# Optimization experiments

Measured on AMD Instinct MI355X. Metric: run time of the kernel, lower is better.

Reference implementation:

```python
import jax, jax.numpy as jnp
import numpy as np

B, NS, NF, T, D = 64, 2, 13, 24, 512
H = 8
DH = D // H
DFF = 2048
EPS = 1e-5


def setup_inputs() -> dict:
    key = jax.random.key(0)
    ks = jax.random.split(key, 16)
    s = 0.02
    inp = {
        'x': jax.random.normal(ks[0], (B, NS * NF, T, D), jnp.float32),
        'w_in_s': jax.random.normal(ks[1], (3 * D, D), jnp.float32) * s,
        'b_in_s': jnp.zeros((3 * D,), jnp.float32),
        'w_out_s': jax.random.normal(ks[2], (D, D), jnp.float32) * s,
        'b_out_s': jnp.zeros((D,), jnp.float32),
        'w_in_f': jax.random.normal(ks[3], (3 * D, D), jnp.float32) * s,
        'b_in_f': jnp.zeros((3 * D,), jnp.float32),
        'w_out_f': jax.random.normal(ks[4], (D, D), jnp.float32) * s,
        'b_out_f': jnp.zeros((D,), jnp.float32),
        'w1': jax.random.normal(ks[5], (DFF, D), jnp.float32) * s,
        'b1': jnp.zeros((DFF,), jnp.float32),
        'w2': jax.random.normal(ks[6], (D, DFF), jnp.float32) * s,
        'b2': jnp.zeros((D,), jnp.float32),
        'g1': jnp.ones((D,), jnp.float32), 'be1': jnp.zeros((D,), jnp.float32),
        'g2': jnp.ones((D,), jnp.float32), 'be2': jnp.zeros((D,), jnp.float32),
        'g3': jnp.ones((D,), jnp.float32), 'be3': jnp.zeros((D,), jnp.float32),
    }
    return inp


def _layer_norm(x, g, b):
    mu = jnp.mean(x, axis=-1, keepdims=True)
    var = jnp.mean(jnp.square(x - mu), axis=-1, keepdims=True)
    return (x - mu) * jax.lax.rsqrt(var + EPS) * g + b


def _mha(x, w_in, b_in, w_out, b_out):
    # x: [..., S, D]; torch nn.MultiheadAttention math, eval mode (no dropout)
    qkv = x @ w_in.T + b_in                     # [..., S, 3D]
    q, k, v = jnp.split(qkv, 3, axis=-1)
    shp = q.shape[:-1] + (H, DH)
    q, k, v = q.reshape(shp), k.reshape(shp), v.reshape(shp)
    scores = jnp.einsum('...qhd,...khd->...hqk', q, k) / np.sqrt(DH).astype(np.float32)
    a = jax.nn.softmax(scores, axis=-1)
    o = jnp.einsum('...hqk,...khd->...qhd', a, v).reshape(x.shape)
    return o @ w_out.T + b_out


def reference(x, w_in_s, b_in_s, w_out_s, b_out_s, w_in_f, b_in_f, w_out_f, b_out_f,
              w1, b1, w2, b2, g1, be1, g2, be2, g3, be3):
    xr = x.reshape(B, NS, NF, T, D)
    # station attention: attend over the NS axis for each (feature, t)
    xs = xr.transpose(0, 2, 3, 1, 4)            # [B, NF, T, NS, D]
    xs = xs + _mha(xs, w_in_s, b_in_s, w_out_s, b_out_s)
    x = xs.transpose(0, 3, 1, 2, 4).reshape(B, NS * NF, T, D)
    x = _layer_norm(x, g1, be1)
    # feature attention: attend over the NF axis for each (station, t)
    xr = x.reshape(B, NS, NF, T, D)
    xf = xr.transpose(0, 1, 3, 2, 4)            # [B, NS, T, NF, D]
    xf = xf + _mha(xf, w_in_f, b_in_f, w_out_f, b_out_f)
    x = xf.transpose(0, 1, 3, 2, 4).reshape(B, NS * NF, T, D)
    x = _layer_norm(x, g2, be2)
    # feed-forward
    ff = jax.nn.relu(x @ w1.T + b1) @ w2.T + b2
    x = _layer_norm(x + ff, g3, be3)
    return x
```

## Files before the change

kernel.cpp:

```cpp
#include <hip/hip_runtime.h>
#include <stdint.h>

typedef unsigned short u16;
typedef __bf16 bf16x8 __attribute__((ext_vector_type(8)));
typedef float f32x4 __attribute__((ext_vector_type(4)));

#define DEV __device__ __forceinline__

DEV float bf2f(u16 u) {
    union { uint32_t u; float f; } c; c.u = ((uint32_t)u) << 16; return c.f;
}
DEV u16 f2bf(float f) {
    union { float f; uint32_t u; } c; c.f = f;
    uint32_t u = c.u;
    u += 0x7FFFu + ((u >> 16) & 1u);
    return (u16)(u >> 16);
}

DEV void gload_lds16(const u16* gp, u16* lp) {
    __builtin_amdgcn_global_load_lds(
        (__attribute__((address_space(1))) u16*)(uintptr_t)gp,
        (__attribute__((address_space(3))) u16*)lp,
        16, 0, 0);
}

#define WAITVM6 asm volatile("s_waitcnt vmcnt(6)" ::: "memory")
#define WAITVM4 asm volatile("s_waitcnt vmcnt(4)" ::: "memory")
#define WAITVM0 asm volatile("s_waitcnt vmcnt(0)" ::: "memory")
#define MEMFENCE asm volatile("" ::: "memory")

DEV void load16f(const u16* p, float* f) {
    uint4 a = *reinterpret_cast<const uint4*>(p);
    uint4 b = *reinterpret_cast<const uint4*>(p + 8);
    uint32_t w[8] = { a.x, a.y, a.z, a.w, b.x, b.y, b.z, b.w };
#pragma unroll
    for (int k = 0; k < 8; ++k) {
        union { uint32_t u; float f; } lo, hi;
        lo.u = w[k] << 16; hi.u = w[k] & 0xFFFF0000u;
        f[2 * k] = lo.f; f[2 * k + 1] = hi.f;
    }
}
DEV float dot16(const u16* p, const float* q) {
    uint4 a = *reinterpret_cast<const uint4*>(p);
    uint4 b = *reinterpret_cast<const uint4*>(p + 8);
    uint32_t w[8] = { a.x, a.y, a.z, a.w, b.x, b.y, b.z, b.w };
    float d = 0.0f;
#pragma unroll
    for (int k = 0; k < 8; ++k) {
        union { uint32_t u; float f; } lo, hi;
        lo.u = w[k] << 16; hi.u = w[k] & 0xFFFF0000u;
        d += q[2 * k] * lo.f;
        d += q[2 * k + 1] * hi.f;
    }
    return d;
}
DEV void fma16(const u16* p, float pw, float* acc) {
    uint4 a = *reinterpret_cast<const uint4*>(p);
    uint4 b = *reinterpret_cast<const uint4*>(p + 8);
    uint32_t w[8] = { a.x, a.y, a.z, a.w, b.x, b.y, b.z, b.w };
#pragma unroll
    for (int k = 0; k < 8; ++k) {
        union { uint32_t u; float f; } lo, hi;
        lo.u = w[k] << 16; hi.u = w[k] & 0xFFFF0000u;
        acc[2 * k] += pw * lo.f;
        acc[2 * k + 1] += pw * hi.f;
    }
}
DEV void store16(u16* p, const float* y) {
    uint32_t w[8];
#pragma unroll
    for (int k = 0; k < 8; ++k)
        w[k] = (uint32_t)f2bf(y[2 * k]) | ((uint32_t)f2bf(y[2 * k + 1]) << 16);
    uint4 a = { w[0], w[1], w[2], w[3] };
    uint4 b = { w[4], w[5], w[6], w[7] };
    *reinterpret_cast<uint4*>(p) = a;
    *reinterpret_cast<uint4*>(p + 8) = b;
}

__global__ __launch_bounds__(256) void k_f32_to_bf16(
    const float* __restrict__ in, u16* __restrict__ out, int n4)
{
    int i = blockIdx.x * 256 + threadIdx.x;
    if (i >= n4) return;
    float4 v = reinterpret_cast<const float4*>(in)[i];
    ushort4 o;
    o.x = f2bf(v.x); o.y = f2bf(v.y); o.z = f2bf(v.z); o.w = f2bf(v.w);
    reinterpret_cast<ushort4*>(out)[i] = o;
}

__global__ __launch_bounds__(256) void k_convw(
    const float* __restrict__ s0, const float* __restrict__ s1,
    const float* __restrict__ s2, const float* __restrict__ s3,
    const float* __restrict__ s4, const float* __restrict__ s5,
    u16* __restrict__ out)
{
    const int i = blockIdx.x * 256 + threadIdx.x;
    const float4* src;
    int off;
    if      (i <  196608) { src = (const float4*)s0; off = i; }
    else if (i <  262144) { src = (const float4*)s1; off = i - 196608; }
    else if (i <  458752) { src = (const float4*)s2; off = i - 262144; }
    else if (i <  524288) { src = (const float4*)s3; off = i - 458752; }
    else if (i <  786432) { src = (const float4*)s4; off = i - 524288; }
    else                  { src = (const float4*)s5; off = i - 786432; }
    float4 v = src[off];
    ushort4 o;
    o.x = f2bf(v.x); o.y = f2bf(v.y); o.z = f2bf(v.z); o.w = f2bf(v.w);
    reinterpret_cast<ushort4*>(out)[i] = o;
}

template<bool RELU, bool RESID, int NT>
__global__ __launch_bounds__(512, 2) void k_gemm8p(
    const u16* __restrict__ A, const u16* __restrict__ W,
    const float* __restrict__ bias, const u16* __restrict__ res,
    u16* __restrict__ C, int M, int N, int K)
{
    __shared__ __align__(16) u16 Abuf[2][16384];
    __shared__ __align__(16) u16 Bbuf[2][16384];

    const int tid  = threadIdx.x;
    const int lane = tid & 63;
    const int wave = tid >> 6;
    const int wm   = wave >> 2;
    const int wn   = wave & 3;
    const int l15  = lane & 15;
    const int lg   = lane >> 4;

    const int nwg = gridDim.x;
    const int v = (blockIdx.x & 7) * (nwg >> 3) + (blockIdx.x >> 3);
    const long tileM = (long)(v / NT) * 256;
    const long tileN = (long)(v % NT) * 256;

    const int nIter = K >> 7;

    f32x4 acc[8][4] = {};

    const long Abase = (tileM + (tid >> 3)) * (long)K + (((tid & 7) ^ ((tid >> 3) & 7)) << 3);
    const long Bbase = (tileN + (tid >> 3)) * (long)K + (((tid & 7) ^ ((tid >> 3) & 7)) << 3);

    auto stA = [&](int h, int t) {
#pragma unroll
        for (int e = 0; e < 2; ++e)
            gload_lds16(A + Abase + (long)(h * 128 + e * 64) * K + t * 64,
                        &Abuf[t & 1][(h * 1024 + e * 512 + tid) * 8]);
    };
    auto stB = [&](int h, int t) {
#pragma unroll
        for (int e = 0; e < 2; ++e)
            gload_lds16(W + Bbase + (long)(h * 128 + e * 64) * K + t * 64,
                        &Bbuf[t & 1][(h * 1024 + e * 512 + tid) * 8]);
    };

    int koff[2];
#pragma unroll
    for (int ks = 0; ks < 2; ++ks)
        koff[ks] = ((ks * 4 + lg) ^ (l15 & 7)) * 8;
    const int aRow = wm * 128 + l15;
    const int bRow = wn * 64 + l15;

    stA(0, 0); stA(1, 0); stB(0, 0); stB(1, 0); stB(0, 1); stB(1, 1);
    WAITVM4;
    MEMFENCE;
    __builtin_amdgcn_s_barrier();
    MEMFENCE;

    bf16x8 b[4][2];

    for (int j = 0; j < nIter; ++j) {
        const bool pre = (j + 1 < nIter);
        const int E = 2 * j;
#pragma unroll
        for (int ph = 0; ph < 8; ++ph) {
            const int bb = ph >> 2;
            const int q  = ph & 3;
            if (q == 0) {
#pragma unroll
                for (int n = 0; n < 4; ++n)
#pragma unroll
                    for (int ks = 0; ks < 2; ++ks)
                        b[n][ks] = *reinterpret_cast<const bf16x8*>(
                            &Bbuf[bb][(bRow + n * 16) * 64 + koff[ks]]);
            }
            bf16x8 aq[2][2];
#pragma unroll
            for (int mi = 0; mi < 2; ++mi)
#pragma unroll
                for (int ks = 0; ks < 2; ++ks)
                    aq[mi][ks] = *reinterpret_cast<const bf16x8*>(
                        &Abuf[bb][(aRow + (q * 2 + mi) * 16) * 64 + koff[ks]]);
            if (ph == 0) stA(0, E + 1);
            else if (ph == 1) stA(1, E + 1);
            else if (ph == 2) { if (pre) stB(0, E + 2); }
            else if (ph == 3) {
                if (pre) { stB(1, E + 2); WAITVM4; } else { WAITVM0; }
            }
            else if (ph == 4) { if (pre) stA(0, E + 2); }
            else if (ph == 5) { if (pre) stA(1, E + 2); }
            else if (ph == 6) { if (pre) stB(0, E + 3); }
            else {
                if (pre) { stB(1, E + 3); WAITVM4; } else { WAITVM0; }
            }
            MEMFENCE;
            __builtin_amdgcn_s_barrier();
            MEMFENCE;
            __builtin_amdgcn_s_setprio(1);
#pragma unroll
            for (int mi = 0; mi < 2; ++mi)
#pragma unroll
                for (int n = 0; n < 4; ++n)
#pragma unroll
                    for (int ks = 0; ks < 2; ++ks)
                        acc[q * 2 + mi][n] = __builtin_amdgcn_mfma_f32_16x16x32_bf16(
                            aq[mi][ks], b[n][ks], acc[q * 2 + mi][n], 0, 0, 0);
            __builtin_amdgcn_s_setprio(0);
            MEMFENCE;
            __builtin_amdgcn_s_barrier();
            MEMFENCE;
        }
    }

    const int crow0 = (int)tileM + wm * 128 + ((lane >> 4) << 2);
    const int ccol0 = (int)tileN + wn * 64 + l15;
#pragma unroll
    for (int m = 0; m < 8; ++m) {
#pragma unroll
        for (int n = 0; n < 4; ++n) {
            const int col = ccol0 + n * 16;
            const float bv = bias[col];
#pragma unroll
            for (int r = 0; r < 4; ++r) {
                const long row = crow0 + m * 16 + r;
                float vv = acc[m][n][r] + bv;
                if (RESID) vv += bf2f(res[row * N + col]);
                if (RELU)  vv = fmaxf(vv, 0.0f);
                C[row * N + col] = f2bf(vv);
            }
        }
    }
}

template<bool RELU, bool RESID, int NT>
__global__ __launch_bounds__(512, 2) void k_gemm3s(
    const u16* __restrict__ A, const u16* __restrict__ W,
    const float* __restrict__ bias, const u16* __restrict__ res,
    u16* __restrict__ C, int M, int N, int K)
{
    __shared__ __align__(16) u16 Abuf[3][16384];
    __shared__ __align__(16) u16 Bbuf[3][8192];

    const int tid  = threadIdx.x;
    const int lane = tid & 63;
    const int wave = tid >> 6;
    const int wm   = wave >> 1;
    const int wn   = wave & 1;
    const int l15  = lane & 15;
    const int lg   = lane >> 4;

    const int nwg = gridDim.x;
    const int v = (blockIdx.x & 7) * (nwg >> 3) + (blockIdx.x >> 3);
    const long tileM = (long)(v / NT) * 256;
    const long tileN = (long)(v % NT) * 128;

    const int nT = K >> 6;

    f32x4 acc[4][4] = {};

    const long Abase = (tileM + (tid >> 3)) * (long)K + (((tid & 7) ^ ((tid >> 3) & 7)) << 3);
    const long Bbase = (tileN + (tid >> 3)) * (long)K + (((tid & 7) ^ ((tid >> 3) & 7)) << 3);

    auto stage = [&](int t, int p) {
        const int s = t % 3;
        const long ko = (long)t * 64;
        if (p == 0) {
#pragma unroll
            for (int e = 0; e < 3; ++e)
                gload_lds16(A + Abase + (long)(e * 64) * K + ko,
                            &Abuf[s][(e * 512 + tid) * 8]);
        } else {
            gload_lds16(A + Abase + (long)192 * K + ko,
                        &Abuf[s][(3 * 512 + tid) * 8]);
#pragma unroll
            for (int e = 0; e < 2; ++e)
                gload_lds16(W + Bbase + (long)(e * 64) * K + ko,
                            &Bbuf[s][(e * 512 + tid) * 8]);
        }
    };

    int koff[2];
#pragma unroll
    for (int ks = 0; ks < 2; ++ks)
        koff[ks] = ((ks * 4 + lg) ^ (l15 & 7)) * 8;
    const int aRow = wm * 64 + l15;
    const int bRow = wn * 64 + l15;

    stage(0, 0); stage(0, 1);
    stage(1, 0); stage(1, 1);
    WAITVM6;
    MEMFENCE;
    __builtin_amdgcn_s_barrier();
    MEMFENCE;

    for (int j = 0; j < nT; ++j) {
        const int s = j % 3;
        const u16* ab = Abuf[s];
        const u16* bb = Bbuf[s];
        const bool pre = (j + 2 < nT);

        bf16x8 bfr[4][2];
#pragma unroll
        for (int n = 0; n < 4; ++n)
#pragma unroll
            for (int ks = 0; ks < 2; ++ks)
                bfr[n][ks] = *reinterpret_cast<const bf16x8*>(
                    &bb[(bRow + n * 16) * 64 + koff[ks]]);
        bf16x8 a0[2][2];
#pragma unroll
        for (int mi = 0; mi < 2; ++mi)
#pragma unroll
            for (int ks = 0; ks < 2; ++ks)
                a0[mi][ks] = *reinterpret_cast<const bf16x8*>(
                    &ab[(aRow + mi * 16) * 64 + koff[ks]]);
        if (pre) stage(j + 2, 0);
        MEMFENCE;
        __builtin_amdgcn_s_barrier();
        MEMFENCE;
        __builtin_amdgcn_s_setprio(1);
#pragma unroll
        for (int mi = 0; mi < 2; ++mi)
#pragma unroll
            for (int n = 0; n < 4; ++n)
#pragma unroll
                for (int ks = 0; ks < 2; ++ks)
                    acc[mi][n] = __builtin_amdgcn_mfma_f32_16x16x32_bf16(
                        a0[mi][ks], bfr[n][ks], acc[mi][n], 0, 0, 0);
        __builtin_amdgcn_s_setprio(0);
        MEMFENCE;
        __builtin_amdgcn_s_barrier();
        MEMFENCE;

        bf16x8 a1[2][2];
#pragma unroll
        for (int mi = 0; mi < 2; ++mi)
#pragma unroll
            for (int ks = 0; ks < 2; ++ks)
                a1[mi][ks] = *reinterpret_cast<const bf16x8*>(
                    &ab[(aRow + (2 + mi) * 16) * 64 + koff[ks]]);
        if (pre) { stage(j + 2, 1); WAITVM6; }
        else if (j + 1 < nT) { WAITVM0; }
        MEMFENCE;
        __builtin_amdgcn_s_barrier();
        MEMFENCE;
        __builtin_amdgcn_s_setprio(1);
#pragma unroll
        for (int mi = 0; mi < 2; ++mi)
#pragma unroll
            for (int n = 0; n < 4; ++n)
#pragma unroll
                for (int ks = 0; ks < 2; ++ks)
                    acc[2 + mi][n] = __builtin_amdgcn_mfma_f32_16x16x32_bf16(
                        a1[mi][ks], bfr[n][ks], acc[2 + mi][n], 0, 0, 0);
        __builtin_amdgcn_s_setprio(0);
        MEMFENCE;
        __builtin_amdgcn_s_barrier();
        MEMFENCE;
    }

    const int crow0 = (int)tileM + wm * 64 + ((lane >> 4) << 2);
    const int ccol0 = (int)tileN + wn * 64 + l15;
#pragma unroll
    for (int m = 0; m < 4; ++m) {
#pragma unroll
        for (int n = 0; n < 4; ++n) {
            const int col = ccol0 + n * 16;
            const float bv = bias[col];
#pragma unroll
            for (int r = 0; r < 4; ++r) {
                const long row = crow0 + m * 16 + r;
                float vv = acc[m][n][r] + bv;
                if (RESID) vv += bf2f(res[row * N + col]);
                if (RELU)  vv = fmaxf(vv, 0.0f);
                C[row * N + col] = f2bf(vv);
            }
        }
    }
}

__global__ __launch_bounds__(256) void k_attn_s(
    const u16* __restrict__ qkv, u16* __restrict__ o)
{
    const int wave = threadIdx.x >> 6, lane = threadIdx.x & 63;
    const int g = blockIdx.x * 4 + wave;
    const int t = g % 24, bf = g / 24, f = bf % 13, b = bf / 13;
    const int base = b * 624 + f * 24 + t;
    const int h = lane >> 3, i = (lane >> 2) & 1, c = lane & 3;
    const int off = h * 64 + c * 16;

    float qf[16];
    load16f(qkv + (size_t)(base + i * 312) * 1536 + off, qf);

    float s[2];
#pragma unroll
    for (int j = 0; j < 2; ++j) {
        float d = dot16(qkv + (size_t)(base + j * 312) * 1536 + 512 + off, qf);
        d += __shfl_xor(d, 1);
        d += __shfl_xor(d, 2);
        s[j] = d * 0.125f;
    }
    const float m = fmaxf(s[0], s[1]);
    const float e0 = expf(s[0] - m), e1 = expf(s[1] - m);
    const float inv = 1.0f / (e0 + e1);
    const float p0 = e0 * inv, p1 = e1 * inv;

    float acc[16] = {};
    fma16(qkv + (size_t)base * 1536 + 1024 + off, p0, acc);
    fma16(qkv + (size_t)(base + 312) * 1536 + 1024 + off, p1, acc);

    store16(o + (size_t)(base + i * 312) * 512 + off, acc);
}

__global__ __launch_bounds__(256) void k_attn_f(
    const u16* __restrict__ qkv, u16* __restrict__ o)
{
    const int wave = threadIdx.x >> 6, lane = threadIdx.x & 63;
    const int p = blockIdx.x * 4 + wave;
    const int h = p & 7, g = p >> 3;
    const int t = g % 24, bs = g / 24, st = bs % 2, b = bs / 2;
    const int base = b * 624 + st * 312 + t;
    const int i = lane >> 2, c = lane & 3;
    const int iq = (i < 13) ? i : 12;
    const int off = h * 64 + c * 16;

    float qf[16];
    load16f(qkv + (size_t)(base + iq * 24) * 1536 + off, qf);

    float sc[13];
#pragma unroll
    for (int j = 0; j < 13; ++j) {
        float d = dot16(qkv + (size_t)(base + j * 24) * 1536 + 512 + off, qf);
        d += __shfl_xor(d, 1);
        d += __shfl_xor(d, 2);
        sc[j] = d * 0.125f;
    }
    float m = sc[0];
#pragma unroll
    for (int j = 1; j < 13; ++j) m = fmaxf(m, sc[j]);
    float den = 0.0f;
#pragma unroll
    for (int j = 0; j < 13; ++j) { sc[j] = expf(sc[j] - m); den += sc[j]; }
    const float inv = 1.0f / den;

    float acc[16] = {};
#pragma unroll
    for (int j = 0; j < 13; ++j)
        fma16(qkv + (size_t)(base + j * 24) * 1536 + 1024 + off, sc[j], acc);
#pragma unroll
    for (int e = 0; e < 16; ++e) acc[e] *= inv;

    if (i < 13)
        store16(o + (size_t)(base + i * 24) * 512 + off, acc);
}

template<bool OUTF32>
__global__ __launch_bounds__(256) void k_ln(
    const u16* __restrict__ in, const float* __restrict__ g,
    const float* __restrict__ be, u16* __restrict__ outb,
    float* __restrict__ outf)
{
    const int row  = blockIdx.x * 4 + (threadIdx.x >> 6);
    const int lane = threadIdx.x & 63;
    const u16* p = in + (size_t)row * 512 + lane * 8;

    uint4 va = *reinterpret_cast<const uint4*>(p);
    uint32_t ua[4] = { va.x, va.y, va.z, va.w };
    float x[8];
#pragma unroll
    for (int i = 0; i < 4; ++i) {
        x[2 * i]     = bf2f((u16)(ua[i] & 0xFFFFu));
        x[2 * i + 1] = bf2f((u16)(ua[i] >> 16));
    }
    float s = 0.f, sq = 0.f;
#pragma unroll
    for (int i = 0; i < 8; ++i) { s += x[i]; sq += x[i] * x[i]; }
#pragma unroll
    for (int off = 32; off; off >>= 1) {
        s  += __shfl_xor(s, off);
        sq += __shfl_xor(sq, off);
    }
    const float mean = s * (1.0f / 512.0f);
    const float var  = sq * (1.0f / 512.0f) - mean * mean;
    const float rstd = rsqrtf(var + 1e-5f);

    const int col = lane * 8;
    float4 g0 = *reinterpret_cast<const float4*>(g + col);
    float4 g1 = *reinterpret_cast<const float4*>(g + col + 4);
    float4 b0 = *reinterpret_cast<const float4*>(be + col);
    float4 b1 = *reinterpret_cast<const float4*>(be + col + 4);
    float gg[8] = { g0.x, g0.y, g0.z, g0.w, g1.x, g1.y, g1.z, g1.w };
    float bb[8] = { b0.x, b0.y, b0.z, b0.w, b1.x, b1.y, b1.z, b1.w };

    float y[8];
#pragma unroll
    for (int i = 0; i < 8; ++i) y[i] = (x[i] - mean) * rstd * gg[i] + bb[i];

    if (OUTF32) {
        float4 o0 = { y[0], y[1], y[2], y[3] };
        float4 o1 = { y[4], y[5], y[6], y[7] };
        reinterpret_cast<float4*>(outf + (size_t)row * 512 + col)[0] = o0;
        reinterpret_cast<float4*>(outf + (size_t)row * 512 + col + 4)[0] = o1;
    } else {
        uint32_t w[4];
#pragma unroll
        for (int i = 0; i < 4; ++i)
            w[i] = (uint32_t)f2bf(y[2 * i]) | ((uint32_t)f2bf(y[2 * i + 1]) << 16);
        uint4 ov = { w[0], w[1], w[2], w[3] };
        *reinterpret_cast<uint4*>(outb + (size_t)row * 512 + col) = ov;
    }
}

extern "C" void kernel_launch(void* const* d_in, const int* in_sizes, int n_in,
                              void* d_out, int out_size, void* d_ws, size_t ws_size,
                              hipStream_t stream)
{
    const float* x       = (const float*)d_in[0];
    const float* w_in_s  = (const float*)d_in[1];
    const float* b_in_s  = (const float*)d_in[2];
    const float* w_out_s = (const float*)d_in[3];
    const float* b_out_s = (const float*)d_in[4];
    const float* w_in_f  = (const float*)d_in[5];
    const float* b_in_f  = (const float*)d_in[6];
    const float* w_out_f = (const float*)d_in[7];
    const float* b_out_f = (const float*)d_in[8];
    const float* w1      = (const float*)d_in[9];
    const float* b1      = (const float*)d_in[10];
    const float* w2      = (const float*)d_in[11];
    const float* b2      = (const float*)d_in[12];
    const float* g1      = (const float*)d_in[13];
    const float* be1     = (const float*)d_in[14];
    const float* g2      = (const float*)d_in[15];
    const float* be2     = (const float*)d_in[16];
    const float* g3      = (const float*)d_in[17];
    const float* be3     = (const float*)d_in[18];

    const int R = 39936;
    u16* xb   = (u16*)d_ws;
    u16* buf1 = xb + (size_t)R * 512;
    u16* obuf = buf1 + (size_t)R * 1536;
    u16* wqs  = buf1 + (size_t)R * 2048;
    u16* wos  = wqs + 1536 * 512;
    u16* wqf  = wos + 512 * 512;
    u16* wof  = wqf + 1536 * 512;
    u16* w1b  = wof + 512 * 512;
    u16* w2b  = w1b + 2048 * 512;

    {
        int n4 = (R * 512) / 4;
        k_f32_to_bf16<<<dim3((n4 + 255) / 256), dim3(256), 0, stream>>>(x, xb, n4);
    }
    k_convw<<<dim3(1048576 / 256), dim3(256), 0, stream>>>(
        w_in_s, w_out_s, w_in_f, w_out_f, w1, w2, wqs);

    const dim3 blk256(256);
    const dim3 blk512(512);

    k_gemm8p<false, false, 6><<<dim3(936), blk512, 0, stream>>>(
        xb, wqs, b_in_s, nullptr, buf1, R, 1536, 512);
    k_attn_s<<<dim3(19968 / 4), blk256, 0, stream>>>(buf1, obuf);
    k_gemm3s<false, true, 4><<<dim3(624), blk512, 0, stream>>>(
        obuf, wos, b_out_s, xb, xb, R, 512, 512);
    k_ln<false><<<dim3(R / 4), blk256, 0, stream>>>(xb, g1, be1, xb, nullptr);

    k_gemm8p<false, false, 6><<<dim3(936), blk512, 0, stream>>>(
        xb, wqf, b_in_f, nullptr, buf1, R, 1536, 512);
    k_attn_f<<<dim3(24576 / 4), blk256, 0, stream>>>(buf1, obuf);
    k_gemm3s<false, true, 4><<<dim3(624), blk512, 0, stream>>>(
        obuf, wof, b_out_f, xb, xb, R, 512, 512);
    k_ln<false><<<dim3(R / 4), blk256, 0, stream>>>(xb, g2, be2, xb, nullptr);

    k_gemm8p<true, false, 8><<<dim3(1248), blk512, 0, stream>>>(
        xb, w1b, b1, nullptr, buf1, R, 2048, 512);
    k_gemm3s<false, true, 4><<<dim3(624), blk512, 0, stream>>>(
        buf1, w2b, b2, xb, xb, R, 512, 2048);
    k_ln<true><<<dim3(R / 4), blk256, 0, stream>>>(xb, g3, be3, nullptr, (float*)d_out);
}
```

Baseline: 615.2 us.

## Add 128x64-tile triple-buffered GEMM kernel for FFN down-projection

Adds a new GEMM kernel with 128x64 output tiles, 256 threads, two blocks per CU, triple-buffered LDS staging with a swizzled layout, and a split A-load schedule interleaved with MFMA phases. It replaces the previous 512-thread GEMM for the K=2048 FFN second projection and launches 2496 blocks instead of 624. The goal is better occupancy and latency hiding on the long-K GEMM. Smaller tiles lower per-block data reuse and add barrier overhead.

```diff
diff --git a/kernel.cpp b/kernel.cpp
--- a/kernel.cpp
+++ b/kernel.cpp
@@ -385,6 +385,152 @@
     }
 }
 
+template<bool RELU, bool RESID, int NT>
+__global__ __launch_bounds__(256, 2) void k_gemm2b(
+    const u16* __restrict__ A, const u16* __restrict__ W,
+    const float* __restrict__ bias, const u16* __restrict__ res,
+    u16* __restrict__ C, int M, int N, int K)
+{
+    __shared__ __align__(16) u16 Abuf[3][8192];
+    __shared__ __align__(16) u16 Bbuf[3][4096];
+
+    const int tid  = threadIdx.x;
+    const int lane = tid & 63;
+    const int wave = tid >> 6;
+    const int wm   = wave >> 1;
+    const int wn   = wave & 1;
+    const int l15  = lane & 15;
+    const int lg   = lane >> 4;
+
+    const int nwg = gridDim.x;
+    const int v = (blockIdx.x & 7) * (nwg >> 3) + (blockIdx.x >> 3);
+    const long tileM = (long)(v / NT) * 128;
+    const long tileN = (long)(v % NT) * 64;
+
+    const int nT = K >> 6;
+
+    f32x4 acc[4][2] = {};
+
+    const long Abase = (tileM + (tid >> 3)) * (long)K + (((tid & 7) ^ ((tid >> 3) & 7)) << 3);
+    const long Bbase = (tileN + (tid >> 3)) * (long)K + (((tid & 7) ^ ((tid >> 3) & 7)) << 3);
+
+    auto stage = [&](int t, int p) {
+        const int s = t % 3;
+        const long ko = (long)t * 64;
+        if (p == 0) {
+#pragma unroll
+            for (int e = 0; e < 3; ++e)
+                gload_lds16(A + Abase + (long)(e * 32) * K + ko,
+                            &Abuf[s][(e * 256 + tid) * 8]);
+        } else {
+            gload_lds16(A + Abase + (long)96 * K + ko,
+                        &Abuf[s][(3 * 256 + tid) * 8]);
+#pragma unroll
+            for (int e = 0; e < 2; ++e)
+                gload_lds16(W + Bbase + (long)(e * 32) * K + ko,
+                            &Bbuf[s][(e * 256 + tid) * 8]);
+        }
+    };
+
+    int koff[2];
+#pragma unroll
+    for (int ks = 0; ks < 2; ++ks)
+        koff[ks] = ((ks * 4 + lg) ^ (l15 & 7)) * 8;
+    const int aRow = wm * 64 + l15;
+    const int bRow = wn * 32 + l15;
+
+    stage(0, 0); stage(0, 1);
+    stage(1, 0); stage(1, 1);
+    WAITVM6;
+    MEMFENCE;
+    __builtin_amdgcn_s_barrier();
+    MEMFENCE;
+
+    for (int j = 0; j < nT; ++j) {
+        const int s = j % 3;
+        const u16* ab = Abuf[s];
+        const u16* bb = Bbuf[s];
+        const bool pre = (j + 2 < nT);
+
+        bf16x8 bfr[2][2];
+#pragma unroll
+        for (int n = 0; n < 2; ++n)
+#pragma unroll
+            for (int ks = 0; ks < 2; ++ks)
+                bfr[n][ks] = *reinterpret_cast<const bf16x8*>(
+                    &bb[(bRow + n * 16) * 64 + koff[ks]]);
+        bf16x8 a0[2][2];
+#pragma unroll
+        for (int mi = 0; mi < 2; ++mi)
+#pragma unroll
+            for (int ks = 0; ks < 2; ++ks)
+                a0[mi][ks] = *reinterpret_cast<const bf16x8*>(
+                    &ab[(aRow + mi * 16) * 64 + koff[ks]]);
+        if (pre) stage(j + 2, 0);
+        MEMFENCE;
+        __builtin_amdgcn_s_barrier();
+        MEMFENCE;
+        __builtin_amdgcn_s_setprio(1);
+#pragma unroll
+        for (int mi = 0; mi < 2; ++mi)
+#pragma unroll
+            for (int n = 0; n < 2; ++n)
+#pragma unroll
+                for (int ks = 0; ks < 2; ++ks)
+                    acc[mi][n] = __builtin_amdgcn_mfma_f32_16x16x32_bf16(
+                        a0[mi][ks], bfr[n][ks], acc[mi][n], 0, 0, 0);
+        __builtin_amdgcn_s_setprio(0);
+        MEMFENCE;
+        __builtin_amdgcn_s_barrier();
+        MEMFENCE;
+
+        bf16x8 a1[2][2];
+#pragma unroll
+        for (int mi = 0; mi < 2; ++mi)
+#pragma unroll
+            for (int ks = 0; ks < 2; ++ks)
+                a1[mi][ks] = *reinterpret_cast<const bf16x8*>(
+                    &ab[(aRow + (2 + mi) * 16) * 64 + koff[ks]]);
+        if (pre) { stage(j + 2, 1); WAITVM6; }
+        else if (j + 1 < nT) { WAITVM0; }
+        MEMFENCE;
+        __builtin_amdgcn_s_barrier();
+        MEMFENCE;
+        __builtin_amdgcn_s_setprio(1);
+#pragma unroll
+        for (int mi = 0; mi < 2; ++mi)
+#pragma unroll
+            for (int n = 0; n < 2; ++n)
+#pragma unroll
+                for (int ks = 0; ks < 2; ++ks)
+                    acc[2 + mi][n] = __builtin_amdgcn_mfma_f32_16x16x32_bf16(
+                        a1[mi][ks], bfr[n][ks], acc[2 + mi][n], 0, 0, 0);
+        __builtin_amdgcn_s_setprio(0);
+        MEMFENCE;
+        __builtin_amdgcn_s_barrier();
+        MEMFENCE;
+    }
+
+    const int crow0 = (int)tileM + wm * 64 + ((lane >> 4) << 2);
+    const int ccol0 = (int)tileN + wn * 32 + l15;
+#pragma unroll
+    for (int m = 0; m < 4; ++m) {
+#pragma unroll
+        for (int n = 0; n < 2; ++n) {
+            const int col = ccol0 + n * 16;
+            const float bv = bias[col];
+#pragma unroll
+            for (int r = 0; r < 4; ++r) {
+                const long row = crow0 + m * 16 + r;
+                float vv = acc[m][n][r] + bv;
+                if (RESID) vv += bf2f(res[row * N + col]);
+                if (RELU)  vv = fmaxf(vv, 0.0f);
+                C[row * N + col] = f2bf(vv);
+            }
+        }
+    }
+}
+
 __global__ __launch_bounds__(256) void k_attn_s(
     const u16* __restrict__ qkv, u16* __restrict__ o)
 {
@@ -578,7 +724,7 @@
 
     k_gemm8p<true, false, 8><<<dim3(1248), blk512, 0, stream>>>(
         xb, w1b, b1, nullptr, buf1, R, 2048, 512);
-    k_gemm3s<false, true, 4><<<dim3(624), blk512, 0, stream>>>(
+    k_gemm2b<false, true, 8><<<dim3(2496), blk256, 0, stream>>>(
         buf1, w2b, b2, xb, xb, R, 512, 2048);
     k_ln<true><<<dim3(R / 4), blk256, 0, stream>>>(xb, g3, be3, nullptr, (float*)d_out);
 }
```

After: 634.6 us. 3.2% more time.

## Fuse attention output projection with residual add and LayerNorm

Applied to the files above, without the earlier changes.

Adds a GEMM kernel whose block owns 64 full rows of the 512-wide output, so it can add bias and residual, reduce row mean and variance across waves through shared memory, and apply LayerNorm in the epilogue. It replaces the separate out-projection GEMM plus LN launches for both attention stages. This removes one launch and one round trip of the activation through memory per stage. In exchange each block stages the whole 512-column weight slice in 128KB of LDS at one block per CU, which lowers occupancy, and computes variance as E[x^2]-mean^2.

```diff
diff --git a/kernel.cpp b/kernel.cpp
--- a/kernel.cpp
+++ b/kernel.cpp
@@ -380,6 +380,165 @@
                 if (RESID) vv += bf2f(res[row * N + col]);
                 if (RELU)  vv = fmaxf(vv, 0.0f);
                 C[row * N + col] = f2bf(vv);
+            }
+        }
+    }
+}
+
+template<bool OUTF32>
+__global__ __launch_bounds__(512, 1) void k_gemmln(
+    const u16* __restrict__ A, const u16* __restrict__ W,
+    const float* __restrict__ bias, const u16* __restrict__ res,
+    const float* __restrict__ g, const float* __restrict__ be,
+    u16* __restrict__ outb, float* __restrict__ outf, int K)
+{
+    __shared__ __align__(16) u16 As[2][4096];
+    __shared__ __align__(16) u16 Bs[2][32768];
+    __shared__ float lnpart[8][64][2];
+    __shared__ float lnstat[64][2];
+
+    const int tid  = threadIdx.x;
+    const int lane = tid & 63;
+    const int wn   = tid >> 6;
+    const int l15  = lane & 15;
+    const int lg   = lane >> 4;
+
+    const int nwg = gridDim.x;
+    const int v = (blockIdx.x & 7) * (nwg >> 3) + (blockIdx.x >> 3);
+    const long tileM = (long)v * 64;
+
+    const int nT = K >> 6;
+
+    f32x4 acc[4][4] = {};
+
+    const long Abase = (tileM + (tid >> 3)) * (long)K + (((tid & 7) ^ ((tid >> 3) & 7)) << 3);
+    const long Bbase = ((long)(tid >> 3)) * K + (((tid & 7) ^ ((tid >> 3) & 7)) << 3);
+
+    auto stage = [&](int buf, int t) {
+        const long ko = (long)t * 64;
+        gload_lds16(A + Abase + ko, &As[buf][tid * 8]);
+#pragma unroll
+        for (int e = 0; e < 8; ++e)
+            gload_lds16(W + Bbase + (long)(e * 64) * K + ko,
+                        &Bs[buf][(e * 512 + tid) * 8]);
+    };
+
+    int koff[2];
+#pragma unroll
+    for (int ks = 0; ks < 2; ++ks)
+        koff[ks] = ((ks * 4 + lg) ^ (l15 & 7)) * 8;
+
+    auto compute = [&](int buf) {
+        bf16x8 a[4][2], b[4][2];
+#pragma unroll
+        for (int m = 0; m < 4; ++m)
+#pragma unroll
+            for (int ks = 0; ks < 2; ++ks)
+                a[m][ks] = *reinterpret_cast<const bf16x8*>(
+                    &As[buf][(m * 16 + l15) * 64 + koff[ks]]);
+#pragma unroll
+        for (int n = 0; n < 4; ++n)
+#pragma unroll
+            for (int ks = 0; ks < 2; ++ks)
+                b[n][ks] = *reinterpret_cast<const bf16x8*>(
+                    &Bs[buf][(wn * 64 + n * 16 + l15) * 64 + koff[ks]]);
+        __builtin_amdgcn_s_setprio(1);
+#pragma unroll
+        for (int m = 0; m < 4; ++m)
+#pragma unroll
+            for (int n = 0; n < 4; ++n)
+#pragma unroll
+                for (int ks = 0; ks < 2; ++ks)
+                    acc[m][n] = __builtin_amdgcn_mfma_f32_16x16x32_bf16(
+                        a[m][ks], b[n][ks], acc[m][n], 0, 0, 0);
+        __builtin_amdgcn_s_setprio(0);
+    };
+
+    stage(0, 0);
+    __syncthreads();
+    int cur = 0;
+    for (int t = 0; t < nT - 1; ++t) {
+        stage(cur ^ 1, t + 1);
+        compute(cur);
+        __syncthreads();
+        cur ^= 1;
+    }
+    compute(cur);
+
+    const int ccol = wn * 64 + l15;
+    float bv[4];
+#pragma unroll
+    for (int n = 0; n < 4; ++n) bv[n] = bias[ccol + n * 16];
+
+    float sp[4][4], sq[4][4];
+#pragma unroll
+    for (int m = 0; m < 4; ++m)
+#pragma unroll
+        for (int r = 0; r < 4; ++r) { sp[m][r] = 0.f; sq[m][r] = 0.f; }
+
+#pragma unroll
+    for (int m = 0; m < 4; ++m) {
+#pragma unroll
+        for (int r = 0; r < 4; ++r) {
+            const long row = tileM + m * 16 + lg * 4 + r;
+#pragma unroll
+            for (int n = 0; n < 4; ++n) {
+                float xv = acc[m][n][r] + bv[n] + bf2f(res[row * 512 + ccol + n * 16]);
+                acc[m][n][r] = xv;
+                sp[m][r] += xv;
+                sq[m][r] += xv * xv;
+            }
+        }
+    }
+#pragma unroll
+    for (int e = 1; e < 16; e <<= 1) {
+#pragma unroll
+        for (int m = 0; m < 4; ++m)
+#pragma unroll
+            for (int r = 0; r < 4; ++r) {
+                sp[m][r] += __shfl_xor(sp[m][r], e);
+                sq[m][r] += __shfl_xor(sq[m][r], e);
+            }
+    }
+    if (l15 == 0) {
+#pragma unroll
+        for (int m = 0; m < 4; ++m)
+#pragma unroll
+            for (int r = 0; r < 4; ++r) {
+                const int rl = m * 16 + lg * 4 + r;
+                lnpart[wn][rl][0] = sp[m][r];
+                lnpart[wn][rl][1] = sq[m][r];
+            }
+    }
+    __syncthreads();
+    if (tid < 64) {
+        float s = 0.f, q = 0.f;
+#pragma unroll
+        for (int w = 0; w < 8; ++w) { s += lnpart[w][tid][0]; q += lnpart[w][tid][1]; }
+        const float mean = s * (1.0f / 512.0f);
+        const float var  = q * (1.0f / 512.0f) - mean * mean;
+        lnstat[tid][0] = mean;
+        lnstat[tid][1] = rsqrtf(var + 1e-5f);
+    }
+    __syncthreads();
+
+    float gv[4], bev[4];
+#pragma unroll
+    for (int n = 0; n < 4; ++n) { gv[n] = g[ccol + n * 16]; bev[n] = be[ccol + n * 16]; }
+
+#pragma unroll
+    for (int m = 0; m < 4; ++m) {
+#pragma unroll
+        for (int r = 0; r < 4; ++r) {
+            const int rl = m * 16 + lg * 4 + r;
+            const float mean = lnstat[rl][0];
+            const float rstd = lnstat[rl][1];
+            const long row = tileM + rl;
+#pragma unroll
+            for (int n = 0; n < 4; ++n) {
+                const float y = (acc[m][n][r] - mean) * rstd * gv[n] + bev[n];
+                if (OUTF32) outf[row * 512 + ccol + n * 16] = y;
+                else        outb[row * 512 + ccol + n * 16] = f2bf(y);
             }
         }
     }
@@ -565,16 +724,14 @@
     k_gemm8p<false, false, 6><<<dim3(936), blk512, 0, stream>>>(
         xb, wqs, b_in_s, nullptr, buf1, R, 1536, 512);
     k_attn_s<<<dim3(19968 / 4), blk256, 0, stream>>>(buf1, obuf);
-    k_gemm3s<false, true, 4><<<dim3(624), blk512, 0, stream>>>(
-        obuf, wos, b_out_s, xb, xb, R, 512, 512);
-    k_ln<false><<<dim3(R / 4), blk256, 0, stream>>>(xb, g1, be1, xb, nullptr);
+    k_gemmln<false><<<dim3(624), blk512, 0, stream>>>(
+        obuf, wos, b_out_s, xb, g1, be1, xb, nullptr, 512);
 
     k_gemm8p<false, false, 6><<<dim3(936), blk512, 0, stream>>>(
         xb, wqf, b_in_f, nullptr, buf1, R, 1536, 512);
     k_attn_f<<<dim3(24576 / 4), blk256, 0, stream>>>(buf1, obuf);
-    k_gemm3s<false, true, 4><<<dim3(624), blk512, 0, stream>>>(
-        obuf, wof, b_out_f, xb, xb, R, 512, 512);
-    k_ln<false><<<dim3(R / 4), blk256, 0, stream>>>(xb, g2, be2, xb, nullptr);
+    k_gemmln<false><<<dim3(624), blk512, 0, stream>>>(
+        obuf, wof, b_out_f, xb, g2, be2, xb, nullptr, 512);
 
     k_gemm8p<true, false, 8><<<dim3(1248), blk512, 0, stream>>>(
         xb, w1b, b1, nullptr, buf1, R, 2048, 512);
```

Measured after the change: 623.0 us. No clear change (+1.3%).
